# Performance work log

Hardware: AMD Instinct MI355X
Metric: run time of the kernel (lower is better)

## Reference

```python
import jax, jax.numpy as jnp
import numpy as np

B, S, D = 2, 2048, 2048
H, KVH = 16, 8
HD = D // H          # 128
REP = H // KVH       # 2
FF = 5504
EPS = 1e-5
THETA = 1e6


def rotate_half(x):
    h = x.shape[-1] // 2
    return jnp.concatenate([-x[..., h:], x[..., :h]], axis=-1)


def rms_norm(x, g):
    v = jnp.mean(x.astype(jnp.float32) ** 2, axis=-1, keepdims=True)
    return (x * jax.lax.rsqrt(v + EPS)).astype(x.dtype) * g


def setup_inputs() -> dict:
    key = jax.random.key(0)
    ks = jax.random.split(key, 10)
    # RoPE tables [S, HD]
    inv_freq = 1.0 / (THETA ** (np.arange(0, HD, 2, dtype=np.float32) / HD))
    t = np.arange(S, dtype=np.float32)
    freqs = np.outer(t, inv_freq)                      # [S, HD/2]
    emb = np.concatenate([freqs, freqs], axis=-1)      # [S, HD]
    sc = 0.02
    return {
        "x": jax.random.normal(ks[0], (B, S, D), jnp.float32),
        "cos": jnp.asarray(np.cos(emb)),
        "sin": jnp.asarray(np.sin(emb)),
        "wq": jax.random.normal(ks[1], (H * HD, D), jnp.float32) * sc,
        "wk": jax.random.normal(ks[2], (KVH * HD, D), jnp.float32) * sc,
        "wv": jax.random.normal(ks[3], (KVH * HD, D), jnp.float32) * sc,
        "wo": jax.random.normal(ks[4], (D, H * HD), jnp.float32) * sc,
        "w_gate": jax.random.normal(ks[5], (FF, D), jnp.float32) * sc,
        "w_up": jax.random.normal(ks[6], (FF, D), jnp.float32) * sc,
        "w_down": jax.random.normal(ks[7], (D, FF), jnp.float32) * sc,
        "g1": jnp.ones((D,), jnp.float32),
        "g2": jnp.ones((D,), jnp.float32),
    }


def reference(x, cos, sin, wq, wk, wv, wo, w_gate, w_up, w_down, g1, g2):
    # ---- attention sub-block ----
    h = rms_norm(x, g1)
    q = (h @ wq.T).reshape(B, S, H, HD)
    k = (h @ wk.T).reshape(B, S, KVH, HD)
    v = (h @ wv.T).reshape(B, S, KVH, HD)
    # RoPE: cos/sin [S,HD] -> broadcast over (B, S, heads, HD) via unsqueeze at head dim
    c = cos[:S][:, None, :]
    s = sin[:S][:, None, :]
    q = q * c + rotate_half(q) * s
    k = k * c + rotate_half(k) * s
    # GQA repeat_kv (repeat_interleave on head dim), then bshd -> bhsd
    k = jnp.repeat(k, REP, axis=2).transpose(0, 2, 1, 3)
    v = jnp.repeat(v, REP, axis=2).transpose(0, 2, 1, 3)
    q = q.transpose(0, 2, 1, 3)
    scores = jnp.einsum("bhqd,bhkd->bhqk", q, k) / jnp.sqrt(jnp.float32(HD))
    causal = jnp.triu(jnp.full((S, S), -jnp.inf, jnp.float32), k=1)
    scores = scores + causal[None, None]
    attn = jax.nn.softmax(scores.astype(jnp.float32), axis=-1).astype(scores.dtype)
    out = jnp.einsum("bhqk,bhkd->bhqd", attn, v)
    out = out.transpose(0, 2, 1, 3).reshape(B, S, H * HD)
    x = x + out @ wo.T
    # ---- SwiGLU MLP sub-block ----
    h2 = rms_norm(x, g2)
    mlp = (jax.nn.silu(h2 @ w_gate.T) * (h2 @ w_up.T)) @ w_down.T
    return x + mlp
```

## Files before the change

kernel.cpp:

```cpp
#include <hip/hip_runtime.h>


#define DM 2048
#define SEQ 2048
#define HD 128
#define FF_ 5504
#define QK_SCALE_L2E 0.12751744f

typedef __bf16 bf16x8 __attribute__((ext_vector_type(8)));
typedef float f32x4 __attribute__((ext_vector_type(4)));
typedef float f32x16 __attribute__((ext_vector_type(16)));
typedef unsigned short u16x8 __attribute__((ext_vector_type(8)));
typedef unsigned int u32x4 __attribute__((ext_vector_type(4)));

typedef __attribute__((address_space(1))) void* gas1;
typedef __attribute__((address_space(3))) void* las3;
#define GLDS16(g, s) __builtin_amdgcn_global_load_lds((gas1)(g), (las3)(s), 16, 0, 0)

static __device__ __forceinline__ float bf2f(unsigned short u) {
  union { unsigned int i; float f; } c; c.i = ((unsigned int)u) << 16; return c.f;
}
static __device__ __forceinline__ unsigned short f2bf(float f) {
  __bf16 b = (__bf16)f;
  return __builtin_bit_cast(unsigned short, b);
}
static __device__ __forceinline__ unsigned int pk2(float a, float b) {
  return (unsigned int)f2bf(a) | ((unsigned int)f2bf(b) << 16);
}
static __device__ __forceinline__ float fexp2(float x) { return exp2f(x); }

__global__ __launch_bounds__(256) void k_conv(const float* __restrict__ src,
                                              unsigned short* __restrict__ dst) {
  size_t i = (size_t)(blockIdx.x * 256 + threadIdx.x) * 8;
  float4 a = *(const float4*)&src[i];
  float4 b = *(const float4*)&src[i + 4];
  u16x8 o;
  o[0] = f2bf(a.x); o[1] = f2bf(a.y); o[2] = f2bf(a.z); o[3] = f2bf(a.w);
  o[4] = f2bf(b.x); o[5] = f2bf(b.y); o[6] = f2bf(b.z); o[7] = f2bf(b.w);
  *(u16x8*)&dst[i] = o;
}

__global__ __launch_bounds__(256) void k_conv_gu(const float* __restrict__ g,
                                                 const float* __restrict__ u,
                                                 unsigned short* __restrict__ dst) {
  int i = blockIdx.x * 256 + threadIdx.x;
  int row = i >> 8;
  int c8 = (i & 255) * 8;
  int t = row >> 8, r = row & 255;
  const float* src = (r < 128) ? (g + (size_t)(t * 128 + r) * DM + c8)
                               : (u + (size_t)(t * 128 + (r - 128)) * DM + c8);
  float4 a = *(const float4*)src;
  float4 b = *(const float4*)(src + 4);
  u16x8 o;
  o[0] = f2bf(a.x); o[1] = f2bf(a.y); o[2] = f2bf(a.z); o[3] = f2bf(a.w);
  o[4] = f2bf(b.x); o[5] = f2bf(b.y); o[6] = f2bf(b.z); o[7] = f2bf(b.w);
  *(u16x8*)&dst[(size_t)row * DM + c8] = o;
}

__global__ __launch_bounds__(256) void k_rmsnorm(const float* __restrict__ x,
                                                 const float* __restrict__ g,
                                                 unsigned short* __restrict__ out) {
  int row = blockIdx.x, tid = threadIdx.x;
  const float* xr = x + (size_t)row * DM;
  float4 a = *(const float4*)&xr[tid * 8];
  float4 b = *(const float4*)&xr[tid * 8 + 4];
  float ss = a.x * a.x + a.y * a.y + a.z * a.z + a.w * a.w +
             b.x * b.x + b.y * b.y + b.z * b.z + b.w * b.w;
#pragma unroll
  for (int off = 32; off > 0; off >>= 1) ss += __shfl_xor(ss, off, 64);
  __shared__ float red[4];
  if ((tid & 63) == 0) red[tid >> 6] = ss;
  __syncthreads();
  float rs = rsqrtf((red[0] + red[1] + red[2] + red[3]) * (1.0f / DM) + 1e-5f);
  float4 ga = *(const float4*)&g[tid * 8];
  float4 gb = *(const float4*)&g[tid * 8 + 4];
  u16x8 o;
  o[0] = f2bf(a.x * rs * ga.x); o[1] = f2bf(a.y * rs * ga.y);
  o[2] = f2bf(a.z * rs * ga.z); o[3] = f2bf(a.w * rs * ga.w);
  o[4] = f2bf(b.x * rs * gb.x); o[5] = f2bf(b.y * rs * gb.y);
  o[6] = f2bf(b.z * rs * gb.z); o[7] = f2bf(b.w * rs * gb.w);
  *(u16x8*)&out[(size_t)row * DM + tid * 8] = o;
}

__global__ __launch_bounds__(256) void k_rope(unsigned short* __restrict__ qkv,
                                              const float* __restrict__ cosT,
                                              const float* __restrict__ sinT) {
  int idx = blockIdx.x * 256 + threadIdx.x;
  int j = idx & 63;
  int hh = (idx >> 6) % 24;
  int tok = idx / (64 * 24);
  int s = tok & (SEQ - 1);
  int colbase = (hh < 16) ? hh * HD : DM + (hh - 16) * HD;
  unsigned short* p = qkv + (size_t)tok * 4096 + colbase;
  float lo = bf2f(p[j]), hi = bf2f(p[j + 64]);
  const float* cr = cosT + (size_t)s * HD;
  const float* sr = sinT + (size_t)s * HD;
  float nl = lo * cr[j] - hi * sr[j];
  float nh = hi * cr[j + 64] + lo * sr[j + 64];
  if (hh < 16) { nl *= QK_SCALE_L2E; nh *= QK_SCALE_L2E; }
  p[j] = f2bf(nl);
  p[j + 64] = f2bf(nh);
}

template <int BN, int EPI>
__global__ __launch_bounds__(512, 2) void k_gemm8(
    const unsigned short* __restrict__ A, const unsigned short* __restrict__ Bt,
    unsigned short* __restrict__ outB, float* __restrict__ outF,
    const float* __restrict__ res, int N, int K) {
  constexpr int NF = BN / 64;
  constexpr int BSTMT = BN / 128;
  constexpr int ABY = 256 * 64;
  constexpr int BBY = BN * 64;
  constexpr int BUF = ABY + BBY;
  constexpr int VPK = 2 + BSTMT;
  __shared__ __attribute__((aligned(16))) unsigned char smem[4 * BUF];

  const int tid = threadIdx.x, w = tid >> 6, l = tid & 63;
  const int wr = w >> 2, wc = w & 3, lr = l & 15, lg = l >> 4;
  const int nwg = gridDim.x, bid = blockIdx.x;
  const int bswz = (bid & 7) * (nwg >> 3) + (bid >> 3);
  const int mt = bswz & 15, nt = bswz >> 4;
  const int m0 = mt * 256, n0 = nt * BN;
  const int nk = K >> 5;

  const int srow = w * 16 + (l >> 2);
  const int sg8 = ((l & 3) ^ ((l >> 3) & 3)) * 8;
  const unsigned short* Asrc = A + (size_t)(m0 + srow) * K + sg8;
  const unsigned short* Bsrc = Bt + (size_t)(n0 + srow) * K + sg8;
  const int aoff = (wr * 128 + lr) * 64 + ((lg ^ ((lr >> 1) & 3)) << 4);
  const int boff = (wc * (BN / 4) + lr) * 64 + ((lg ^ ((lr >> 1) & 3)) << 4);

  auto stageA = [&](int kt) {
    unsigned char* bb = smem + (kt & 3) * BUF;
#pragma unroll
    for (int i = 0; i < 2; i++)
      GLDS16(Asrc + (size_t)i * 128 * K + kt * 32, bb + (i * 512 + w * 64) * 16);
  };
  auto stageB = [&](int kt) {
    unsigned char* bb = smem + (kt & 3) * BUF + ABY;
#pragma unroll
    for (int i = 0; i < BSTMT; i++)
      GLDS16(Bsrc + (size_t)i * 128 * K + kt * 32, bb + (i * 512 + w * 64) * 16);
  };

  f32x4 acc[8][NF] = {};

  for (int kt = 0; kt < 3; kt++) { stageA(kt); stageB(kt); }
  asm volatile("s_waitcnt vmcnt(%0)" ::"i"(2 * VPK) : "memory");
  __builtin_amdgcn_s_barrier();

  for (int kt = 0; kt < nk; kt++) {
    unsigned char* ba = smem + (kt & 3) * BUF;
    unsigned char* bb = ba + ABY;
    const bool st = (kt + 3) < nk;
    if constexpr (BN == 256) {
      bf16x8 am[4], bnf[4];
#pragma unroll
      for (int m = 0; m < 4; m++) am[m] = *(const bf16x8*)(ba + aoff + m * 1024);
#pragma unroll
      for (int n = 0; n < 4; n++) bnf[n] = *(const bf16x8*)(bb + boff + n * 1024);
      if (st) stageA(kt + 3);
      __builtin_amdgcn_s_barrier();
      __builtin_amdgcn_s_setprio(1);
#pragma unroll
      for (int m = 0; m < 4; m++)
#pragma unroll
        for (int n = 0; n < 4; n++)
          acc[m][n] = __builtin_amdgcn_mfma_f32_16x16x32_bf16(am[m], bnf[n], acc[m][n], 0, 0, 0);
      __builtin_amdgcn_s_setprio(0);
      __builtin_amdgcn_s_barrier();
#pragma unroll
      for (int m = 0; m < 4; m++) am[m] = *(const bf16x8*)(ba + aoff + (m + 4) * 1024);
      if (st) stageB(kt + 3);
      __builtin_amdgcn_s_barrier();
      __builtin_amdgcn_s_setprio(1);
#pragma unroll
      for (int m = 0; m < 4; m++)
#pragma unroll
        for (int n = 0; n < 4; n++)
          acc[m + 4][n] = __builtin_amdgcn_mfma_f32_16x16x32_bf16(am[m], bnf[n], acc[m + 4][n], 0, 0, 0);
      __builtin_amdgcn_s_setprio(0);
      if (kt <= nk - 4)      asm volatile("s_waitcnt vmcnt(%0)" ::"i"(2 * VPK) : "memory");
      else if (kt == nk - 3) asm volatile("s_waitcnt vmcnt(%0)" ::"i"(VPK) : "memory");
      else if (kt == nk - 2) asm volatile("s_waitcnt vmcnt(0)" ::: "memory");
      __builtin_amdgcn_s_barrier();
    } else {
      bf16x8 am[8], bnf[2];
#pragma unroll
      for (int m = 0; m < 8; m++) am[m] = *(const bf16x8*)(ba + aoff + m * 1024);
#pragma unroll
      for (int n = 0; n < 2; n++) bnf[n] = *(const bf16x8*)(bb + boff + n * 1024);
      if (st) { stageA(kt + 3); stageB(kt + 3); }
      __builtin_amdgcn_s_barrier();
      __builtin_amdgcn_s_setprio(1);
#pragma unroll
      for (int m = 0; m < 8; m++)
#pragma unroll
        for (int n = 0; n < 2; n++)
          acc[m][n] = __builtin_amdgcn_mfma_f32_16x16x32_bf16(am[m], bnf[n], acc[m][n], 0, 0, 0);
      __builtin_amdgcn_s_setprio(0);
      if (kt <= nk - 4)      asm volatile("s_waitcnt vmcnt(%0)" ::"i"(2 * VPK) : "memory");
      else if (kt == nk - 3) asm volatile("s_waitcnt vmcnt(%0)" ::"i"(VPK) : "memory");
      else if (kt == nk - 2) asm volatile("s_waitcnt vmcnt(0)" ::: "memory");
      __builtin_amdgcn_s_barrier();
    }
  }

  const int rbase = wr * 128 + lg * 4;
  const int cbase = wc * (BN / 4) + lr;
  if constexpr (EPI == 0) {
#pragma unroll
    for (int m = 0; m < 8; m++)
#pragma unroll
      for (int n = 0; n < NF; n++)
#pragma unroll
        for (int j = 0; j < 4; j++)
          outB[(size_t)(m0 + rbase + m * 16 + j) * N + n0 + cbase + n * 16] =
              f2bf(acc[m][n][j]);
  } else if constexpr (EPI == 1) {
#pragma unroll
    for (int m = 0; m < 8; m++)
#pragma unroll
      for (int n = 0; n < NF; n++)
#pragma unroll
        for (int j = 0; j < 4; j++) {
          size_t o = (size_t)(m0 + rbase + m * 16 + j) * N + n0 + cbase + n * 16;
          outF[o] = res[o] + acc[m][n][j];
        }
  } else {
    float* gl = (float*)smem;
    if (wc < 2) {
#pragma unroll
      for (int m = 0; m < 8; m++)
#pragma unroll
        for (int n = 0; n < NF; n++)
#pragma unroll
          for (int j = 0; j < 4; j++)
            gl[(rbase + m * 16 + j) * 128 + wc * 64 + n * 16 + lr] = acc[m][n][j];
    }
    __syncthreads();
    if (wc >= 2) {
      const int ab = n0 >> 1;
#pragma unroll
      for (int m = 0; m < 8; m++)
#pragma unroll
        for (int n = 0; n < NF; n++)
#pragma unroll
          for (int j = 0; j < 4; j++) {
            int rl = rbase + m * 16 + j;
            int cl = (wc - 2) * 64 + n * 16 + lr;
            float g = gl[rl * 128 + cl];
            float s = g / (1.0f + __expf(-g));
            outB[(size_t)(m0 + rl) * FF_ + ab + cl] = f2bf(s * acc[m][n][j]);
          }
    }
  }
}

__global__ __launch_bounds__(256) void k_attn2(const unsigned short* __restrict__ qkv,
                                               unsigned short* __restrict__ out) {
  __shared__ __attribute__((aligned(16))) unsigned short lK[2][64 * 128];
  __shared__ __attribute__((aligned(16))) unsigned short lV[2][128 * 64];
  const float NEG = -3.0e38f;
  int bx = blockIdx.x;
  int qtile = 15 - (bx >> 5);
  int hb = bx & 31;
  int h = hb & 15, b = hb >> 4;
  int q0 = qtile * 128;
  int tid = threadIdx.x, w = tid >> 6, l = tid & 63;
  int l31 = l & 31, half2 = l >> 5;
  const unsigned short* base = qkv + (size_t)b * SEQ * 4096;
  const unsigned short* Kp = base + 2048 + (h >> 1) * HD;
  const unsigned short* Vp = base + 3072 + (h >> 1) * HD;
  const int qw = q0 + w * 32;

  bf16x8 qf[8];
  {
    const unsigned short* qrow = base + (size_t)(qw + l31) * 4096 + h * HD + half2 * 8;
#pragma unroll
    for (int d = 0; d < 8; d++) qf[d] = *(const bf16x8*)(qrow + d * 16);
  }

  f32x16 oacc[4] = {};
  float mrow = NEG, lsum = 0.0f;

  const int vp = tid & 31, vdc = tid >> 5;
  u16x8 va0, va1, vb0, vb1;

  auto stageK = [&](int t) {
    unsigned char* dst = (unsigned char*)lK[t & 1];
#pragma unroll
    for (int i = 0; i < 4; i++) {
      int c = i * 256 + tid;
      int row = c >> 4;
      int g = (c & 15) ^ (row & 7);
      GLDS16(Kp + (size_t)(t * 64 + row) * 4096 + g * 8, dst + (i * 256 + w * 64) * 16);
    }
  };
  auto loadV = [&](int t) {
    const unsigned short* vr = Vp + (size_t)(t * 64 + vp * 2) * 4096 + vdc * 16;
    va0 = *(const u16x8*)(vr);
    va1 = *(const u16x8*)(vr + 8);
    vb0 = *(const u16x8*)(vr + 4096);
    vb1 = *(const u16x8*)(vr + 4096 + 8);
  };

  const int nt = (q0 >> 6) + 2;
  stageK(0);
  loadV(0);

  for (int t = 0; t < nt; t++) {
    __syncthreads();
    {
      unsigned char* lv = (unsigned char*)lV[t & 1];
#pragma unroll
      for (int j = 0; j < 16; j++) {
        int dd = vdc * 16 + j;
        unsigned short lo = (j < 8) ? va0[j] : va1[j - 8];
        unsigned short hi = (j < 8) ? vb0[j] : vb1[j - 8];
        unsigned int pkv = (unsigned int)lo | ((unsigned int)hi << 16);
        *(unsigned int*)(lv + dd * 128 + (((vp >> 2) ^ (dd & 7)) * 16) + (vp & 3) * 4) = pkv;
      }
    }
    __syncthreads();
    if (t + 1 < nt) { stageK(t + 1); loadV(t + 1); }
    const int kv0 = t * 64;
    if (kv0 <= qw + 31) {
      f32x16 sc[2] = {};
      const unsigned char* lk = (const unsigned char*)lK[t & 1];
#pragma unroll
      for (int hh = 0; hh < 2; hh++) {
        int kk = hh * 32 + l31;
        const unsigned char* krow = lk + kk * 256;
#pragma unroll
        for (int d = 0; d < 8; d++) {
          bf16x8 kf = *(const bf16x8*)(krow + (((d * 2 + half2) ^ (kk & 7)) * 16));
          sc[hh] = __builtin_amdgcn_mfma_f32_32x32x16_bf16(kf, qf[d], sc[hh], 0, 0, 0);
        }
      }
      const int qa = qw + l31;
      if (kv0 + 63 > qw) {
#pragma unroll
        for (int hh = 0; hh < 2; hh++)
#pragma unroll
          for (int r = 0; r < 16; r++) {
            int kva = kv0 + hh * 32 + (r & 3) + 8 * (r >> 2) + 4 * half2;
            if (kva > qa) sc[hh][r] = NEG;
          }
      }
      float mx = sc[0][0];
#pragma unroll
      for (int r = 1; r < 16; r++) mx = fmaxf(mx, sc[0][r]);
#pragma unroll
      for (int r = 0; r < 16; r++) mx = fmaxf(mx, sc[1][r]);
      mx = fmaxf(mx, __shfl_xor(mx, 32));
      bool ok = (mx <= mrow + 11.0f);
      if (__ballot(ok) != ~0ull) {
        float mnew = fmaxf(mrow, mx);
        float fct = fexp2(mrow - mnew);
        mrow = mnew;
        lsum *= fct;
#pragma unroll
        for (int r = 0; r < 16; r++) {
          int rr = (r & 3) + 8 * (r >> 2) + 4 * half2;
          float fr = __shfl(fct, rr);
#pragma unroll
          for (int d = 0; d < 4; d++) oacc[d][r] *= fr;
        }
      }
      float ps = 0.0f;
#pragma unroll
      for (int hh = 0; hh < 2; hh++)
#pragma unroll
        for (int r = 0; r < 16; r++) {
          float e = fexp2(sc[hh][r] - mrow);
          sc[hh][r] = e;
          ps += e;
        }
      ps += __shfl_xor(ps, 32);
      lsum += ps;
      const unsigned char* lv = (const unsigned char*)lV[t & 1];
#pragma unroll
      for (int s = 0; s < 4; s++) {
        const int hh = s >> 1;
        const int r0 = (s & 1) * 8;
        unsigned int lo0, lo1, hi0, hi1;
        if (hh == 0) {
          lo0 = pk2(sc[0][r0 + 0], sc[0][r0 + 1]); lo1 = pk2(sc[0][r0 + 2], sc[0][r0 + 3]);
          hi0 = pk2(sc[0][r0 + 4], sc[0][r0 + 5]); hi1 = pk2(sc[0][r0 + 6], sc[0][r0 + 7]);
        } else {
          lo0 = pk2(sc[1][r0 + 0], sc[1][r0 + 1]); lo1 = pk2(sc[1][r0 + 2], sc[1][r0 + 3]);
          hi0 = pk2(sc[1][r0 + 4], sc[1][r0 + 5]); hi1 = pk2(sc[1][r0 + 6], sc[1][r0 + 7]);
        }
        unsigned int s0 = half2 ? lo0 : hi0, s1 = half2 ? lo1 : hi1;
        unsigned int rc0 = (unsigned int)__shfl_xor((int)s0, 32);
        unsigned int rc1 = (unsigned int)__shfl_xor((int)s1, 32);
        u32x4 fr;
        fr[0] = half2 ? rc0 : lo0; fr[1] = half2 ? rc1 : lo1;
        fr[2] = half2 ? hi0 : rc0; fr[3] = half2 ? hi1 : rc1;
        bf16x8 pa = __builtin_bit_cast(bf16x8, fr);
#pragma unroll
        for (int d = 0; d < 4; d++) {
          int dd = d * 32 + l31;
          bf16x8 vf = *(const bf16x8*)(lv + dd * 128 + (((s * 2 + half2) ^ (dd & 7)) * 16));
          oacc[d] = __builtin_amdgcn_mfma_f32_32x32x16_bf16(pa, vf, oacc[d], 0, 0, 0);
        }
      }
    }
  }
  float inv = 1.0f / lsum;
#pragma unroll
  for (int r = 0; r < 16; r++) {
    int rr = (r & 3) + 8 * (r >> 2) + 4 * half2;
    float ir = __shfl(inv, rr);
    size_t ob = ((size_t)(b * SEQ + qw + rr)) * 2048 + h * HD;
#pragma unroll
    for (int d = 0; d < 4; d++)
      out[ob + d * 32 + l31] = f2bf(oacc[d][r] * ir);
  }
}

extern "C" void kernel_launch(void* const* d_in, const int* in_sizes, int n_in,
                              void* d_out, int out_size, void* d_ws, size_t ws_size,
                              hipStream_t stream) {
  const float* x = (const float*)d_in[0];
  const float* cosT = (const float*)d_in[1];
  const float* sinT = (const float*)d_in[2];
  const float* wq = (const float*)d_in[3];
  const float* wk = (const float*)d_in[4];
  const float* wv = (const float*)d_in[5];
  const float* wo = (const float*)d_in[6];
  const float* wg = (const float*)d_in[7];
  const float* wu = (const float*)d_in[8];
  const float* wd = (const float*)d_in[9];
  const float* g1 = (const float*)d_in[10];
  const float* g2 = (const float*)d_in[11];
  float* out = (float*)d_out;
  char* ws = (char*)d_ws;

  unsigned short* wqkv = (unsigned short*)(ws + 0);
  unsigned short* hbuf = (unsigned short*)(ws + 16777216);
  unsigned short* qkv = (unsigned short*)(ws + 33554432);
  unsigned short* attn_o = (unsigned short*)(ws + 67108864);
  unsigned short* wo_bf = (unsigned short*)(ws + 83886080);
  unsigned short* wgu = (unsigned short*)(ws + 33554432);
  unsigned short* act = (unsigned short*)(ws + 92274688);
  unsigned short* wdown = (unsigned short*)(ws + 0);

  k_conv<<<2048, 256, 0, stream>>>(wq, wqkv);
  k_conv<<<1024, 256, 0, stream>>>(wk, wqkv + 4194304);
  k_conv<<<1024, 256, 0, stream>>>(wv, wqkv + 6291456);
  k_rmsnorm<<<4096, 256, 0, stream>>>(x, g1, hbuf);
  k_gemm8<256, 0><<<256, 512, 0, stream>>>(hbuf, wqkv, qkv, nullptr, nullptr,
                                           4096, 2048);
  k_rope<<<24576, 256, 0, stream>>>(qkv, cosT, sinT);
  k_attn2<<<512, 256, 0, stream>>>(qkv, attn_o);
  k_conv<<<2048, 256, 0, stream>>>(wo, wo_bf);
  k_gemm8<128, 1><<<256, 512, 0, stream>>>(attn_o, wo_bf, nullptr, out, x,
                                           2048, 2048);
  k_rmsnorm<<<4096, 256, 0, stream>>>(out, g2, hbuf);
  k_conv_gu<<<11008, 256, 0, stream>>>(wg, wu, wgu);
  k_gemm8<256, 2><<<688, 512, 0, stream>>>(hbuf, wgu, act, nullptr, nullptr,
                                           11008, 2048);
  k_conv<<<5504, 256, 0, stream>>>(wd, wdown);
  k_gemm8<128, 1><<<256, 512, 0, stream>>>(act, wdown, nullptr, out, out,
                                           2048, 5504);
}
```

Measured before the change: 613.9 us.

## Load GEMM B fragments directly to registers and shrink LDS to A only

The GEMM kernel no longer stages the weight (B) tile through LDS. Each wave loads its B fragments straight from global memory into registers, double-buffered with a one-step prefetch, while A keeps its 4-stage LDS pipeline. The loop is unrolled by two with explicit vmcnt waits and one barrier per k-step, and the LDS footprint drops to 64KB, which may raise occupancy. The SwiGLU epilogue is split into two row halves so it fits in the smaller LDS. The cost is redundant global and L2 traffic, since waves sharing B columns each load them, plus more registers.

Measured after the change: 691.4 us. +12.6%, slower.

```diff
diff --git a/kernel.cpp b/kernel.cpp
--- a/kernel.cpp
+++ b/kernel.cpp
@@ -28,6 +28,9 @@
   return (unsigned int)f2bf(a) | ((unsigned int)f2bf(b) << 16);
 }
 static __device__ __forceinline__ float fexp2(float x) { return exp2f(x); }
+static __device__ __forceinline__ void ldg_b128(u32x4& dst, const unsigned short* p) {
+  asm volatile("global_load_dwordx4 %0, %1, off" : "=v"(dst) : "v"(p));
+}
 
 __global__ __launch_bounds__(256) void k_conv(const float* __restrict__ src,
                                               unsigned short* __restrict__ dst) {
@@ -108,12 +111,7 @@
     unsigned short* __restrict__ outB, float* __restrict__ outF,
     const float* __restrict__ res, int N, int K) {
   constexpr int NF = BN / 64;
-  constexpr int BSTMT = BN / 128;
-  constexpr int ABY = 256 * 64;
-  constexpr int BBY = BN * 64;
-  constexpr int BUF = ABY + BBY;
-  constexpr int VPK = 2 + BSTMT;
-  __shared__ __attribute__((aligned(16))) unsigned char smem[4 * BUF];
+  __shared__ __attribute__((aligned(16))) unsigned char smem[4 * 16384];
 
   const int tid = threadIdx.x, w = tid >> 6, l = tid & 63;
   const int wr = w >> 2, wc = w & 3, lr = l & 15, lg = l >> 4;
@@ -126,85 +124,56 @@
   const int srow = w * 16 + (l >> 2);
   const int sg8 = ((l & 3) ^ ((l >> 3) & 3)) * 8;
   const unsigned short* Asrc = A + (size_t)(m0 + srow) * K + sg8;
-  const unsigned short* Bsrc = Bt + (size_t)(n0 + srow) * K + sg8;
   const int aoff = (wr * 128 + lr) * 64 + ((lg ^ ((lr >> 1) & 3)) << 4);
-  const int boff = (wc * (BN / 4) + lr) * 64 + ((lg ^ ((lr >> 1) & 3)) << 4);
+  const unsigned short* Bb = Bt + (size_t)(n0 + wc * (BN / 4) + lr) * K + lg * 8;
 
   auto stageA = [&](int kt) {
-    unsigned char* bb = smem + (kt & 3) * BUF;
+    unsigned char* bb = smem + (kt & 3) * 16384;
 #pragma unroll
     for (int i = 0; i < 2; i++)
       GLDS16(Asrc + (size_t)i * 128 * K + kt * 32, bb + (i * 512 + w * 64) * 16);
   };
-  auto stageB = [&](int kt) {
-    unsigned char* bb = smem + (kt & 3) * BUF + ABY;
-#pragma unroll
-    for (int i = 0; i < BSTMT; i++)
-      GLDS16(Bsrc + (size_t)i * 128 * K + kt * 32, bb + (i * 512 + w * 64) * 16);
-  };
 
   f32x4 acc[8][NF] = {};
-
-  for (int kt = 0; kt < 3; kt++) { stageA(kt); stageB(kt); }
-  asm volatile("s_waitcnt vmcnt(%0)" ::"i"(2 * VPK) : "memory");
+  u32x4 b0[NF], b1[NF];
+
+#pragma unroll
+  for (int n = 0; n < NF; n++) ldg_b128(b0[n], Bb + (size_t)n * 16 * K);
+  stageA(0); stageA(1); stageA(2);
+  asm volatile("s_waitcnt vmcnt(4)" ::: "memory");
   __builtin_amdgcn_s_barrier();
 
-  for (int kt = 0; kt < nk; kt++) {
-    unsigned char* ba = smem + (kt & 3) * BUF;
-    unsigned char* bb = ba + ABY;
-    const bool st = (kt + 3) < nk;
-    if constexpr (BN == 256) {
-      bf16x8 am[4], bnf[4];
-#pragma unroll
-      for (int m = 0; m < 4; m++) am[m] = *(const bf16x8*)(ba + aoff + m * 1024);
-#pragma unroll
-      for (int n = 0; n < 4; n++) bnf[n] = *(const bf16x8*)(bb + boff + n * 1024);
-      if (st) stageA(kt + 3);
-      __builtin_amdgcn_s_barrier();
-      __builtin_amdgcn_s_setprio(1);
-#pragma unroll
-      for (int m = 0; m < 4; m++)
-#pragma unroll
-        for (int n = 0; n < 4; n++)
-          acc[m][n] = __builtin_amdgcn_mfma_f32_16x16x32_bf16(am[m], bnf[n], acc[m][n], 0, 0, 0);
-      __builtin_amdgcn_s_setprio(0);
-      __builtin_amdgcn_s_barrier();
-#pragma unroll
-      for (int m = 0; m < 4; m++) am[m] = *(const bf16x8*)(ba + aoff + (m + 4) * 1024);
-      if (st) stageB(kt + 3);
-      __builtin_amdgcn_s_barrier();
-      __builtin_amdgcn_s_setprio(1);
-#pragma unroll
-      for (int m = 0; m < 4; m++)
-#pragma unroll
-        for (int n = 0; n < 4; n++)
-          acc[m + 4][n] = __builtin_amdgcn_mfma_f32_16x16x32_bf16(am[m], bnf[n], acc[m + 4][n], 0, 0, 0);
-      __builtin_amdgcn_s_setprio(0);
-      if (kt <= nk - 4)      asm volatile("s_waitcnt vmcnt(%0)" ::"i"(2 * VPK) : "memory");
-      else if (kt == nk - 3) asm volatile("s_waitcnt vmcnt(%0)" ::"i"(VPK) : "memory");
-      else if (kt == nk - 2) asm volatile("s_waitcnt vmcnt(0)" ::: "memory");
-      __builtin_amdgcn_s_barrier();
-    } else {
-      bf16x8 am[8], bnf[2];
-#pragma unroll
-      for (int m = 0; m < 8; m++) am[m] = *(const bf16x8*)(ba + aoff + m * 1024);
-#pragma unroll
-      for (int n = 0; n < 2; n++) bnf[n] = *(const bf16x8*)(bb + boff + n * 1024);
-      if (st) { stageA(kt + 3); stageB(kt + 3); }
-      __builtin_amdgcn_s_barrier();
-      __builtin_amdgcn_s_setprio(1);
-#pragma unroll
-      for (int m = 0; m < 8; m++)
-#pragma unroll
-        for (int n = 0; n < 2; n++)
-          acc[m][n] = __builtin_amdgcn_mfma_f32_16x16x32_bf16(am[m], bnf[n], acc[m][n], 0, 0, 0);
-      __builtin_amdgcn_s_setprio(0);
-      if (kt <= nk - 4)      asm volatile("s_waitcnt vmcnt(%0)" ::"i"(2 * VPK) : "memory");
-      else if (kt == nk - 3) asm volatile("s_waitcnt vmcnt(%0)" ::"i"(VPK) : "memory");
-      else if (kt == nk - 2) asm volatile("s_waitcnt vmcnt(0)" ::: "memory");
-      __builtin_amdgcn_s_barrier();
-    }
-  }
+#define GBODY(KT, CUR, NXT, W)                                                    \
+  {                                                                               \
+    unsigned char* ba = smem + ((KT) & 3) * 16384;                                \
+    bf16x8 am[8];                                                                 \
+    _Pragma("unroll") for (int m = 0; m < 8; m++)                                 \
+        am[m] = *(const bf16x8*)(ba + aoff + m * 1024);                           \
+    if ((KT) + 1 < nk) {                                                          \
+      _Pragma("unroll") for (int n = 0; n < NF; n++)                              \
+          ldg_b128(NXT[n], Bb + (size_t)n * 16 * K + ((KT) + 1) * 32);            \
+    }                                                                             \
+    if ((KT) + 3 < nk) stageA((KT) + 3);                                          \
+    asm volatile("s_waitcnt vmcnt(%0)" ::"i"(W) : "memory");                      \
+    __builtin_amdgcn_sched_barrier(0);                                            \
+    __builtin_amdgcn_s_setprio(1);                                                \
+    _Pragma("unroll") for (int m = 0; m < 8; m++)                                 \
+      _Pragma("unroll") for (int n = 0; n < NF; n++)                              \
+          acc[m][n] = __builtin_amdgcn_mfma_f32_16x16x32_bf16(                    \
+              am[m], __builtin_bit_cast(bf16x8, CUR[n]), acc[m][n], 0, 0, 0);     \
+    __builtin_amdgcn_s_setprio(0);                                                \
+    __builtin_amdgcn_s_barrier();                                                 \
+  }
+
+  for (int kt = 0; kt < nk - 4; kt += 2) {
+    GBODY(kt, b0, b1, NF + 4);
+    GBODY(kt + 1, b1, b0, NF + 4);
+  }
+  GBODY(nk - 4, b0, b1, NF + 4);
+  GBODY(nk - 3, b1, b0, NF + 2);
+  GBODY(nk - 2, b0, b1, NF);
+  GBODY(nk - 1, b1, b0, 0);
+#undef GBODY
 
   const int rbase = wr * 128 + lg * 4;
   const int cbase = wc * (BN / 4) + lr;
@@ -229,30 +198,34 @@
         }
   } else {
     float* gl = (float*)smem;
-    if (wc < 2) {
-#pragma unroll
-      for (int m = 0; m < 8; m++)
-#pragma unroll
-        for (int n = 0; n < NF; n++)
-#pragma unroll
-          for (int j = 0; j < 4; j++)
-            gl[(rbase + m * 16 + j) * 128 + wc * 64 + n * 16 + lr] = acc[m][n][j];
-    }
-    __syncthreads();
-    if (wc >= 2) {
-      const int ab = n0 >> 1;
-#pragma unroll
-      for (int m = 0; m < 8; m++)
-#pragma unroll
-        for (int n = 0; n < NF; n++)
-#pragma unroll
-          for (int j = 0; j < 4; j++) {
-            int rl = rbase + m * 16 + j;
-            int cl = (wc - 2) * 64 + n * 16 + lr;
-            float g = gl[rl * 128 + cl];
-            float s = g / (1.0f + __expf(-g));
-            outB[(size_t)(m0 + rl) * FF_ + ab + cl] = f2bf(s * acc[m][n][j]);
-          }
+    const int ab = n0 >> 1;
+#pragma unroll
+    for (int half = 0; half < 2; half++) {
+      if (wr == half && wc < 2) {
+#pragma unroll
+        for (int m = 0; m < 8; m++)
+#pragma unroll
+          for (int n = 0; n < NF; n++)
+#pragma unroll
+            for (int j = 0; j < 4; j++)
+              gl[(m * 16 + lg * 4 + j) * 128 + wc * 64 + n * 16 + lr] = acc[m][n][j];
+      }
+      __syncthreads();
+      if (wr == half && wc >= 2) {
+#pragma unroll
+        for (int m = 0; m < 8; m++)
+#pragma unroll
+          for (int n = 0; n < NF; n++)
+#pragma unroll
+            for (int j = 0; j < 4; j++) {
+              int rl = m * 16 + lg * 4 + j;
+              int cl = (wc - 2) * 64 + n * 16 + lr;
+              float g = gl[rl * 128 + cl];
+              float s = g / (1.0f + __expf(-g));
+              outB[(size_t)(m0 + half * 128 + rl) * FF_ + ab + cl] = f2bf(s * acc[m][n][j]);
+            }
+      }
+      __syncthreads();
     }
   }
 }
```

## Add double-buffered GEMM mode so two workgroups fit per CU

Applied to the files above, without the earlier changes.

Adds a PIPE template mode to the bf16 GEMM that uses two LDS stages instead of four, with a simple prefetch-next-tile loop and a full vmcnt wait per iteration. The SwiGLU epilogue now stages gate values through LDS in two row halves, so its scratch fits in the smaller allocation. The QKV projection moves to 128-wide N tiles with twice as many blocks, and both it and the gate/up GEMM use the new mode. The aim is to raise occupancy by cutting LDS per workgroup, at the cost of shallower prefetch and more exposed global-load latency per K step.

Measured after the change: 623.3 us. Within noise of the previous version (+1.5%).

```diff
diff --git a/kernel.cpp b/kernel.cpp
--- a/kernel.cpp
+++ b/kernel.cpp
@@ -102,7 +102,7 @@
   p[j + 64] = f2bf(nh);
 }
 
-template <int BN, int EPI>
+template <int BN, int EPI, int PIPE>
 __global__ __launch_bounds__(512, 2) void k_gemm8(
     const unsigned short* __restrict__ A, const unsigned short* __restrict__ Bt,
     unsigned short* __restrict__ outB, float* __restrict__ outF,
@@ -113,7 +113,8 @@
   constexpr int BBY = BN * 64;
   constexpr int BUF = ABY + BBY;
   constexpr int VPK = 2 + BSTMT;
-  __shared__ __attribute__((aligned(16))) unsigned char smem[4 * BUF];
+  constexpr int NBUF = PIPE ? 2 : 4;
+  __shared__ __attribute__((aligned(16))) unsigned char smem[NBUF * BUF];
 
   const int tid = threadIdx.x, w = tid >> 6, l = tid & 63;
   const int wr = w >> 2, wc = w & 3, lr = l & 15, lg = l >> 4;
@@ -131,13 +132,13 @@
   const int boff = (wc * (BN / 4) + lr) * 64 + ((lg ^ ((lr >> 1) & 3)) << 4);
 
   auto stageA = [&](int kt) {
-    unsigned char* bb = smem + (kt & 3) * BUF;
+    unsigned char* bb = smem + (kt & (NBUF - 1)) * BUF;
 #pragma unroll
     for (int i = 0; i < 2; i++)
       GLDS16(Asrc + (size_t)i * 128 * K + kt * 32, bb + (i * 512 + w * 64) * 16);
   };
   auto stageB = [&](int kt) {
-    unsigned char* bb = smem + (kt & 3) * BUF + ABY;
+    unsigned char* bb = smem + (kt & (NBUF - 1)) * BUF + ABY;
 #pragma unroll
     for (int i = 0; i < BSTMT; i++)
       GLDS16(Bsrc + (size_t)i * 128 * K + kt * 32, bb + (i * 512 + w * 64) * 16);
@@ -145,58 +146,49 @@
 
   f32x4 acc[8][NF] = {};
 
-  for (int kt = 0; kt < 3; kt++) { stageA(kt); stageB(kt); }
-  asm volatile("s_waitcnt vmcnt(%0)" ::"i"(2 * VPK) : "memory");
-  __builtin_amdgcn_s_barrier();
-
-  for (int kt = 0; kt < nk; kt++) {
-    unsigned char* ba = smem + (kt & 3) * BUF;
-    unsigned char* bb = ba + ABY;
-    const bool st = (kt + 3) < nk;
-    if constexpr (BN == 256) {
-      bf16x8 am[4], bnf[4];
-#pragma unroll
-      for (int m = 0; m < 4; m++) am[m] = *(const bf16x8*)(ba + aoff + m * 1024);
-#pragma unroll
-      for (int n = 0; n < 4; n++) bnf[n] = *(const bf16x8*)(bb + boff + n * 1024);
-      if (st) stageA(kt + 3);
-      __builtin_amdgcn_s_barrier();
+  if constexpr (PIPE == 1) {
+    stageA(0); stageB(0);
+    asm volatile("s_waitcnt vmcnt(0)" ::: "memory");
+    __builtin_amdgcn_s_barrier();
+    for (int kt = 0; kt < nk; kt++) {
+      unsigned char* ba = smem + (kt & 1) * BUF;
+      unsigned char* bb = ba + ABY;
+      if (kt + 1 < nk) { stageA(kt + 1); stageB(kt + 1); }
+      bf16x8 am[8], bnf[NF];
+#pragma unroll
+      for (int m = 0; m < 8; m++) am[m] = *(const bf16x8*)(ba + aoff + m * 1024);
+#pragma unroll
+      for (int n = 0; n < NF; n++) bnf[n] = *(const bf16x8*)(bb + boff + n * 1024);
       __builtin_amdgcn_s_setprio(1);
 #pragma unroll
-      for (int m = 0; m < 4; m++)
-#pragma unroll
-        for (int n = 0; n < 4; n++)
+      for (int m = 0; m < 8; m++)
+#pragma unroll
+        for (int n = 0; n < NF; n++)
           acc[m][n] = __builtin_amdgcn_mfma_f32_16x16x32_bf16(am[m], bnf[n], acc[m][n], 0, 0, 0);
       __builtin_amdgcn_s_setprio(0);
+      asm volatile("s_waitcnt vmcnt(0)" ::: "memory");
       __builtin_amdgcn_s_barrier();
-#pragma unroll
-      for (int m = 0; m < 4; m++) am[m] = *(const bf16x8*)(ba + aoff + (m + 4) * 1024);
-      if (st) stageB(kt + 3);
-      __builtin_amdgcn_s_barrier();
-      __builtin_amdgcn_s_setprio(1);
-#pragma unroll
-      for (int m = 0; m < 4; m++)
-#pragma unroll
-        for (int n = 0; n < 4; n++)
-          acc[m + 4][n] = __builtin_amdgcn_mfma_f32_16x16x32_bf16(am[m], bnf[n], acc[m + 4][n], 0, 0, 0);
-      __builtin_amdgcn_s_setprio(0);
-      if (kt <= nk - 4)      asm volatile("s_waitcnt vmcnt(%0)" ::"i"(2 * VPK) : "memory");
-      else if (kt == nk - 3) asm volatile("s_waitcnt vmcnt(%0)" ::"i"(VPK) : "memory");
-      else if (kt == nk - 2) asm volatile("s_waitcnt vmcnt(0)" ::: "memory");
-      __builtin_amdgcn_s_barrier();
-    } else {
-      bf16x8 am[8], bnf[2];
+    }
+  } else {
+    for (int kt = 0; kt < 3; kt++) { stageA(kt); stageB(kt); }
+    asm volatile("s_waitcnt vmcnt(%0)" ::"i"(2 * VPK) : "memory");
+    __builtin_amdgcn_s_barrier();
+    for (int kt = 0; kt < nk; kt++) {
+      unsigned char* ba = smem + (kt & 3) * BUF;
+      unsigned char* bb = ba + ABY;
+      const bool st = (kt + 3) < nk;
+      bf16x8 am[8], bnf[NF];
 #pragma unroll
       for (int m = 0; m < 8; m++) am[m] = *(const bf16x8*)(ba + aoff + m * 1024);
 #pragma unroll
-      for (int n = 0; n < 2; n++) bnf[n] = *(const bf16x8*)(bb + boff + n * 1024);
+      for (int n = 0; n < NF; n++) bnf[n] = *(const bf16x8*)(bb + boff + n * 1024);
       if (st) { stageA(kt + 3); stageB(kt + 3); }
       __builtin_amdgcn_s_barrier();
       __builtin_amdgcn_s_setprio(1);
 #pragma unroll
       for (int m = 0; m < 8; m++)
 #pragma unroll
-        for (int n = 0; n < 2; n++)
+        for (int n = 0; n < NF; n++)
           acc[m][n] = __builtin_amdgcn_mfma_f32_16x16x32_bf16(am[m], bnf[n], acc[m][n], 0, 0, 0);
       __builtin_amdgcn_s_setprio(0);
       if (kt <= nk - 4)      asm volatile("s_waitcnt vmcnt(%0)" ::"i"(2 * VPK) : "memory");
@@ -229,30 +221,35 @@
         }
   } else {
     float* gl = (float*)smem;
-    if (wc < 2) {
-#pragma unroll
-      for (int m = 0; m < 8; m++)
-#pragma unroll
-        for (int n = 0; n < NF; n++)
-#pragma unroll
-          for (int j = 0; j < 4; j++)
-            gl[(rbase + m * 16 + j) * 128 + wc * 64 + n * 16 + lr] = acc[m][n][j];
-    }
+    const int ab = n0 >> 1;
     __syncthreads();
-    if (wc >= 2) {
-      const int ab = n0 >> 1;
-#pragma unroll
-      for (int m = 0; m < 8; m++)
-#pragma unroll
-        for (int n = 0; n < NF; n++)
-#pragma unroll
-          for (int j = 0; j < 4; j++) {
-            int rl = rbase + m * 16 + j;
-            int cl = (wc - 2) * 64 + n * 16 + lr;
-            float g = gl[rl * 128 + cl];
-            float s = g / (1.0f + __expf(-g));
-            outB[(size_t)(m0 + rl) * FF_ + ab + cl] = f2bf(s * acc[m][n][j]);
-          }
+#pragma unroll
+    for (int half = 0; half < 2; half++) {
+      if (wr == half && wc < 2) {
+#pragma unroll
+        for (int m = 0; m < 8; m++)
+#pragma unroll
+          for (int n = 0; n < NF; n++)
+#pragma unroll
+            for (int j = 0; j < 4; j++)
+              gl[(m * 16 + lg * 4 + j) * 128 + wc * 64 + n * 16 + lr] = acc[m][n][j];
+      }
+      __syncthreads();
+      if (wr == half && wc >= 2) {
+#pragma unroll
+        for (int m = 0; m < 8; m++)
+#pragma unroll
+          for (int n = 0; n < NF; n++)
+#pragma unroll
+            for (int j = 0; j < 4; j++) {
+              int rl = m * 16 + lg * 4 + j;
+              int cl = (wc - 2) * 64 + n * 16 + lr;
+              float g = gl[rl * 128 + cl];
+              float s = g / (1.0f + __expf(-g));
+              outB[(size_t)(m0 + half * 128 + rl) * FF_ + ab + cl] = f2bf(s * acc[m][n][j]);
+            }
+      }
+      __syncthreads();
     }
   }
 }
@@ -451,18 +448,18 @@
   k_conv<<<1024, 256, 0, stream>>>(wk, wqkv + 4194304);
   k_conv<<<1024, 256, 0, stream>>>(wv, wqkv + 6291456);
   k_rmsnorm<<<4096, 256, 0, stream>>>(x, g1, hbuf);
-  k_gemm8<256, 0><<<256, 512, 0, stream>>>(hbuf, wqkv, qkv, nullptr, nullptr,
-                                           4096, 2048);
+  k_gemm8<128, 0, 1><<<512, 512, 0, stream>>>(hbuf, wqkv, qkv, nullptr, nullptr,
+                                              4096, 2048);
   k_rope<<<24576, 256, 0, stream>>>(qkv, cosT, sinT);
   k_attn2<<<512, 256, 0, stream>>>(qkv, attn_o);
   k_conv<<<2048, 256, 0, stream>>>(wo, wo_bf);
-  k_gemm8<128, 1><<<256, 512, 0, stream>>>(attn_o, wo_bf, nullptr, out, x,
-                                           2048, 2048);
+  k_gemm8<128, 1, 0><<<256, 512, 0, stream>>>(attn_o, wo_bf, nullptr, out, x,
+                                              2048, 2048);
   k_rmsnorm<<<4096, 256, 0, stream>>>(out, g2, hbuf);
   k_conv_gu<<<11008, 256, 0, stream>>>(wg, wu, wgu);
-  k_gemm8<256, 2><<<688, 512, 0, stream>>>(hbuf, wgu, act, nullptr, nullptr,
-                                           11008, 2048);
+  k_gemm8<256, 2, 1><<<688, 512, 0, stream>>>(hbuf, wgu, act, nullptr, nullptr,
+                                              11008, 2048);
   k_conv<<<5504, 256, 0, stream>>>(wd, wdown);
-  k_gemm8<128, 1><<<256, 512, 0, stream>>>(act, wdown, nullptr, out, out,
-                                           2048, 5504);
-}
+  k_gemm8<128, 1, 0><<<256, 512, 0, stream>>>(act, wdown, nullptr, out, out,
+                                              2048, 5504);
+}
```
